# Optimization experiments

Hardware: AMD Instinct MI355X
Metric: run time of the kernel (lower is better)

Reference implementation:

```python
import jax, jax.numpy as jnp
import numpy as np

B, S, D = 2, 2048, 1024
H, DK = 16, 64  # num_heads, key_dim (value_dim defaults to key_dim)


def setup_inputs() -> dict:
    key = jax.random.key(0)
    ks = jax.random.split(key, 11)
    init = lambda k, shape, fan_in: jax.random.uniform(
        k, shape, jnp.float32, -1.0, 1.0) * (1.0 / np.sqrt(fan_in))
    return {
        "query": jax.random.normal(ks[0], (B, S, D), jnp.float32),
        "key": jax.random.normal(ks[1], (B, S, D), jnp.float32),
        "value": jax.random.normal(ks[2], (B, S, D), jnp.float32),
        "Wq": init(ks[3], (D, H, DK), D),
        "bq": jnp.zeros((H, DK), jnp.float32),
        "Wk": init(ks[4], (D, H, DK), D),
        "bk": jnp.zeros((H, DK), jnp.float32),
        "Wv": init(ks[5], (D, H, DK), D),
        "bv": jnp.zeros((H, DK), jnp.float32),
        "Wo": init(ks[6], (H, DK, D), H * DK),
        "bo": jnp.zeros((D,), jnp.float32),
    }


def reference(query, key, value, Wq, bq, Wk, bk, Wv, bv, Wo, bo):
    # QKV projections: abc,cde->abde (EinsumDense with bias on (H, DK))
    q = jnp.einsum("bsd,dhk->bshk", query, Wq) + bq  # [B,S,H,DK]
    k = jnp.einsum("bsd,dhk->bshk", key, Wk) + bk
    v = jnp.einsum("bsd,dhk->bshk", value, Wv) + bv
    # Keras scales the query before the dot product
    q = q * (1.0 / jnp.sqrt(jnp.asarray(DK, q.dtype)))
    # aecd,abcd->acbe : [B,H,Sq,Sk]
    scores = jnp.einsum("bqhk,bshk->bhqs", q, k)
    probs = jax.nn.softmax(scores, axis=-1)
    # acbe,aecd->abcd : [B,Sq,H,DK]
    attn = jnp.einsum("bhqs,bshk->bqhk", probs, v)
    # output projection: abcd,cde->abe
    out = jnp.einsum("bqhk,hkd->bqd", attn, Wo) + bo  # [B,S,D]
    return out
```

## Files before the change

### kernel.cpp

```cpp
#include <hip/hip_runtime.h>
#include <hip/hip_bf16.h>
#include <stdint.h>
#include <stddef.h>


typedef __bf16 bf16;
typedef __attribute__((ext_vector_type(4))) bf16 bf16x4;
typedef __attribute__((ext_vector_type(8))) bf16 bf16x8;
typedef __attribute__((ext_vector_type(4))) float f32x4;
typedef __attribute__((ext_vector_type(16))) float f32x16;
typedef __attribute__((ext_vector_type(2))) unsigned int uint2v;

#define DEVINL static __device__ __forceinline__

DEVINL void gload_lds16(const void* g, void* l) {
  __builtin_amdgcn_global_load_lds(
      (const __attribute__((address_space(1))) void*)g,
      (__attribute__((address_space(3))) void*)l, 16, 0, 0);
}

DEVINL f32x4 mfma16(bf16x8 a, bf16x8 b, f32x4 c) {
  return __builtin_amdgcn_mfma_f32_16x16x32_bf16(a, b, c, 0, 0, 0);
}
DEVINL f32x16 mfma32(bf16x8 a, bf16x8 b, f32x16 c) {
  return __builtin_amdgcn_mfma_f32_32x32x16_bf16(a, b, c, 0, 0, 0);
}
DEVINL float fexp2(float x) {
  float r;
  asm("v_exp_f32 %0, %1" : "=v"(r) : "v"(x));
  return r;
}
DEVINL unsigned pack2(float lo, float hi) {
  union { bf16 h[2]; unsigned u; } t;
  t.h[0] = (bf16)lo; t.h[1] = (bf16)hi;
  return t.u;
}
DEVINL bf16x8 mk8(unsigned a, unsigned b, unsigned c, unsigned d) {
  union { unsigned u[4]; bf16x8 v; } t;
  t.u[0] = a; t.u[1] = b; t.u[2] = c; t.u[3] = d;
  return t.v;
}

__global__ __launch_bounds__(256) void wt_kernel(
    const float* __restrict__ w0, const float* __restrict__ w1,
    const float* __restrict__ w2, const float* __restrict__ w3,
    bf16* __restrict__ out) {
  __shared__ float tile[64 * 65];
  int t = blockIdx.y;
  const float* w = (t == 0) ? w0 : (t == 1) ? w1 : (t == 2) ? w2 : w3;
  bf16* o = out + (size_t)t * 1024 * 1024;
  int tb = blockIdx.x;
  int k0 = (tb >> 4) * 64, n0 = (tb & 15) * 64;
  int c = threadIdx.x & 63, r0 = threadIdx.x >> 6;
  for (int r = r0; r < 64; r += 4)
    tile[r * 65 + c] = w[(size_t)(k0 + r) * 1024 + n0 + c];
  __syncthreads();
  for (int r = r0; r < 64; r += 4)
    o[(size_t)(n0 + r) * 1024 + k0 + c] = (bf16)tile[c * 65 + r];
}

__global__ __launch_bounds__(256) void cvt_kernel(
    const float* __restrict__ q, const float* __restrict__ k,
    const float* __restrict__ v, bf16* __restrict__ out) {
  int z = blockIdx.y;
  const float* src = (z == 0) ? q : (z == 1) ? k : v;
  size_t off = ((size_t)blockIdx.x * 256 + threadIdx.x) * 8;
  f32x4 a = *(const f32x4*)(src + off);
  f32x4 b = *(const f32x4*)(src + off + 4);
  bf16x8 h;
#pragma unroll
  for (int j = 0; j < 4; ++j) { h[j] = (bf16)a[j]; h[4 + j] = (bf16)b[j]; }
  *(bf16x8*)(out + (size_t)z * 4194304 + off) = h;
}

__global__ __launch_bounds__(256) void gemm_qkv(
    const bf16* __restrict__ Abf, const bf16* __restrict__ Wt,
    const float* __restrict__ bq, const float* __restrict__ bk,
    const float* __restrict__ bv,
    bf16* __restrict__ outQ, bf16* __restrict__ outK, bf16* __restrict__ Vt) {
  int z = blockIdx.z;
  const bf16* A    = Abf + (size_t)z * 4194304;
  const bf16* Wz   = Wt + (size_t)z * 1024 * 1024;
  const float* bia = (z == 0) ? bq : (z == 1) ? bk : bv;
  float scale      = (z == 0) ? 0.18033688011112042f : 1.0f;

  __shared__ bf16 As[2][128 * 32];
  __shared__ bf16 Bs[2][128 * 32];

  int m0 = blockIdx.x * 128, n0 = blockIdx.y * 128;
  int tid = threadIdx.x, w = tid >> 6, l = tid & 63;
  int wm = (w >> 1) * 64, wn = (w & 1) * 64;
  int c16 = l & 15, g = l >> 4;
  int rsw = (c16 >> 1) & 3;

  int brow0 = (w * 2 + 0) * 16 + (l >> 2);
  int brow1 = (w * 2 + 1) * 16 + (l >> 2);
  int bk0 = ((l & 3) ^ ((brow0 >> 1) & 3)) * 8;
  int bk1 = ((l & 3) ^ ((brow1 >> 1) & 3)) * 8;

  f32x4 acc[4][4] = {};

#define STAGE_QKV(buf, kt)                                                   \
  do {                                                                       \
    gload_lds16(A + (size_t)(m0 + brow0) * 1024 + (kt) + bk0,                \
                (char*)As[buf] + (w * 2 + 0) * 1024 + l * 16);               \
    gload_lds16(A + (size_t)(m0 + brow1) * 1024 + (kt) + bk1,                \
                (char*)As[buf] + (w * 2 + 1) * 1024 + l * 16);               \
    gload_lds16(Wz + (size_t)(n0 + brow0) * 1024 + (kt) + bk0,               \
                (char*)Bs[buf] + (w * 2 + 0) * 1024 + l * 16);               \
    gload_lds16(Wz + (size_t)(n0 + brow1) * 1024 + (kt) + bk1,               \
                (char*)Bs[buf] + (w * 2 + 1) * 1024 + l * 16);               \
  } while (0)

  STAGE_QKV(0, 0);
  __syncthreads();

  int cur = 0;
  for (int kt = 0; kt < 1024; kt += 32) {
    if (kt < 992) STAGE_QKV(cur ^ 1, kt + 32);
    bf16x8 af[4], bfr[4];
#pragma unroll
    for (int mt = 0; mt < 4; ++mt)
      af[mt] = *(const bf16x8*)&As[cur][(wm + mt * 16 + c16) * 32 + ((g ^ rsw) * 8)];
#pragma unroll
    for (int nt = 0; nt < 4; ++nt)
      bfr[nt] = *(const bf16x8*)&Bs[cur][(wn + nt * 16 + c16) * 32 + ((g ^ rsw) * 8)];
#pragma unroll
    for (int mt = 0; mt < 4; ++mt)
#pragma unroll
      for (int nt = 0; nt < 4; ++nt)
        acc[mt][nt] = mfma16(af[mt], bfr[nt], acc[mt][nt]);
    __syncthreads();
    cur ^= 1;
  }
#undef STAGE_QKV

  if (z < 2) {
    bf16* Cout = (z == 0) ? outQ : outK;
#pragma unroll
    for (int mt = 0; mt < 4; ++mt)
#pragma unroll
      for (int nt = 0; nt < 4; ++nt) {
        int n = n0 + wn + nt * 16 + c16;
        float bb = bia[n];
#pragma unroll
        for (int r = 0; r < 4; ++r) {
          int m = m0 + wm + mt * 16 + g * 4 + r;
          Cout[(size_t)m * 1024 + n] = (bf16)((acc[mt][nt][r] + bb) * scale);
        }
      }
  } else {
#pragma unroll
    for (int mt = 0; mt < 4; ++mt)
#pragma unroll
      for (int nt = 0; nt < 4; ++nt) {
        int n = n0 + wn + nt * 16 + c16;
        float bb = bia[n];
        int m = m0 + wm + mt * 16 + g * 4;
        int b = m >> 11, s = m & 2047;
        bf16x4 v;
#pragma unroll
        for (int r = 0; r < 4; ++r) v[r] = (bf16)(acc[mt][nt][r] + bb);
        *(bf16x4*)&Vt[((size_t)(b * 16 + (n >> 6)) * 64 + (n & 63)) * 2048 + s] = v;
      }
  }
}

__global__ __launch_bounds__(256) void flash_kernel(
    const bf16* __restrict__ Qp, const bf16* __restrict__ Kp,
    const bf16* __restrict__ Vt, bf16* __restrict__ AO) {
  __shared__ __align__(16) bf16 Ks[2][64 * 64];
  __shared__ __align__(16) bf16 Vs[2][64 * 64];

  int orig = blockIdx.x;
  int wg = (orig & 7) * 64 + (orig >> 3);
  int bh = wg >> 4, qb = wg & 15;
  int b = bh >> 4, h = bh & 15;
  int tid = threadIdx.x, w = tid >> 6, l = tid & 63;
  int lo5 = l & 31, g = l >> 5;
  int q0 = qb * 128 + w * 32;

  const bf16* qptr = Qp + (size_t)(b * 2048 + q0 + lo5) * 1024 + h * 64 + g * 8;
  bf16x8 qf0 = *(const bf16x8*)(qptr + 0);
  bf16x8 qf1 = *(const bf16x8*)(qptr + 16);
  bf16x8 qf2 = *(const bf16x8*)(qptr + 32);
  bf16x8 qf3 = *(const bf16x8*)(qptr + 48);

  const bf16* kbase = Kp + (size_t)(b * 2048) * 1024 + h * 64;
  const bf16* vbase = Vt + (size_t)bh * 64 * 2048;

  int u0 = w * 64 + l;
  int u1 = (4 + w) * 64 + l;
  int r0s = u0 >> 3, c0s = (u0 & 7) ^ (r0s & 7);
  int r1s = u1 >> 3, c1s = (u1 & 7) ^ (r1s & 7);

#define STAGE(buf, s0)                                                          \
  do {                                                                          \
    gload_lds16(kbase + (size_t)((s0) + r0s) * 1024 + c0s * 8,                  \
                (bf16*)Ks[buf] + u0 * 8);                                       \
    gload_lds16(kbase + (size_t)((s0) + r1s) * 1024 + c1s * 8,                  \
                (bf16*)Ks[buf] + u1 * 8);                                       \
    gload_lds16(vbase + (size_t)r0s * 2048 + (s0) + c0s * 8,                    \
                (bf16*)Vs[buf] + u0 * 8);                                       \
    gload_lds16(vbase + (size_t)r1s * 2048 + (s0) + c1s * 8,                    \
                (bf16*)Vs[buf] + u1 * 8);                                       \
  } while (0)

#define LDSK(cp, nt, kt) \
  (*(const bf16x8*)&cp[(((nt)*32 + lo5) << 6) + (((((kt)*2 + g)) ^ (lo5 & 7)) << 3)])
#define LDSV(cp, dt, st) \
  (*(const bf16x8*)&cp[(((dt)*32 + lo5) << 6) + (((((st)*2 + g)) ^ (lo5 & 7)) << 3)])

  f32x16 o0 = {}, o1 = {};
  float ps0 = 0.f, ps1 = 0.f, ps2 = 0.f, ps3 = 0.f;

  STAGE(0, 0);
  int cur = 0;
  for (int t = 0; t < 32; ++t) {
    if (t < 31) {
      STAGE(cur ^ 1, (t + 1) * 64);
      asm volatile("s_waitcnt vmcnt(4)" ::: "memory");
    } else {
      asm volatile("s_waitcnt vmcnt(0)" ::: "memory");
    }
    __builtin_amdgcn_s_barrier();
    __builtin_amdgcn_sched_barrier(0);
    const bf16* kc = Ks[cur];
    const bf16* vc = Vs[cur];

    f32x16 sv = {};
    __builtin_amdgcn_s_setprio(1);
    sv = mfma32(LDSK(kc, 0, 0), qf0, sv);
    sv = mfma32(LDSK(kc, 0, 1), qf1, sv);
    sv = mfma32(LDSK(kc, 0, 2), qf2, sv);
    sv = mfma32(LDSK(kc, 0, 3), qf3, sv);
    __builtin_amdgcn_s_setprio(0);
    float p[16];
#pragma unroll
    for (int r = 0; r < 16; ++r) p[r] = fexp2(sv[r]);
    ps0 += p[0] + p[4] + p[8] + p[12];
    ps1 += p[1] + p[5] + p[9] + p[13];
    ps2 += p[2] + p[6] + p[10] + p[14];
    ps3 += p[3] + p[7] + p[11] + p[15];
    unsigned pw0 = pack2(p[0], p[1]), pw1 = pack2(p[2], p[3]);
    unsigned pw2 = pack2(p[4], p[5]), pw3 = pack2(p[6], p[7]);
    unsigned pw4 = pack2(p[8], p[9]), pw5 = pack2(p[10], p[11]);
    unsigned pw6 = pack2(p[12], p[13]), pw7 = pack2(p[14], p[15]);
    uint2v a02 = __builtin_amdgcn_permlane32_swap(pw0, pw2, false, false);
    uint2v a13 = __builtin_amdgcn_permlane32_swap(pw1, pw3, false, false);
    uint2v a46 = __builtin_amdgcn_permlane32_swap(pw4, pw6, false, false);
    uint2v a57 = __builtin_amdgcn_permlane32_swap(pw5, pw7, false, false);
    bf16x8 pa0 = mk8(a02.x, a13.x, a02.y, a13.y);
    bf16x8 pa1 = mk8(a46.x, a57.x, a46.y, a57.y);

    f32x16 sw = {};
    __builtin_amdgcn_s_setprio(1);
    sw = mfma32(LDSK(kc, 1, 0), qf0, sw);
    sw = mfma32(LDSK(kc, 1, 1), qf1, sw);
    sw = mfma32(LDSK(kc, 1, 2), qf2, sw);
    sw = mfma32(LDSK(kc, 1, 3), qf3, sw);
    __builtin_amdgcn_s_setprio(0);
#pragma unroll
    for (int r = 0; r < 16; ++r) p[r] = fexp2(sw[r]);
    ps0 += p[0] + p[4] + p[8] + p[12];
    ps1 += p[1] + p[5] + p[9] + p[13];
    ps2 += p[2] + p[6] + p[10] + p[14];
    ps3 += p[3] + p[7] + p[11] + p[15];
    pw0 = pack2(p[0], p[1]); pw1 = pack2(p[2], p[3]);
    pw2 = pack2(p[4], p[5]); pw3 = pack2(p[6], p[7]);
    pw4 = pack2(p[8], p[9]); pw5 = pack2(p[10], p[11]);
    pw6 = pack2(p[12], p[13]); pw7 = pack2(p[14], p[15]);
    a02 = __builtin_amdgcn_permlane32_swap(pw0, pw2, false, false);
    a13 = __builtin_amdgcn_permlane32_swap(pw1, pw3, false, false);
    a46 = __builtin_amdgcn_permlane32_swap(pw4, pw6, false, false);
    a57 = __builtin_amdgcn_permlane32_swap(pw5, pw7, false, false);
    bf16x8 pb0 = mk8(a02.x, a13.x, a02.y, a13.y);
    bf16x8 pb1 = mk8(a46.x, a57.x, a46.y, a57.y);

    __builtin_amdgcn_s_setprio(1);
    o0 = mfma32(pa0, LDSV(vc, 0, 0), o0);
    o1 = mfma32(pa0, LDSV(vc, 1, 0), o1);
    o0 = mfma32(pa1, LDSV(vc, 0, 1), o0);
    o1 = mfma32(pa1, LDSV(vc, 1, 1), o1);
    o0 = mfma32(pb0, LDSV(vc, 0, 2), o0);
    o1 = mfma32(pb0, LDSV(vc, 1, 2), o1);
    o0 = mfma32(pb1, LDSV(vc, 0, 3), o0);
    o1 = mfma32(pb1, LDSV(vc, 1, 3), o1);
    __builtin_amdgcn_s_setprio(0);

    __builtin_amdgcn_sched_barrier(0);
    __builtin_amdgcn_s_barrier();
    cur ^= 1;
  }
#undef STAGE
#undef LDSK
#undef LDSV

  float plsum = (ps0 + ps1) + (ps2 + ps3);
  float tot = plsum + __shfl_xor(plsum, 32);

#pragma unroll
  for (int r = 0; r < 16; ++r) {
    int qr = (r & 3) + 8 * (r >> 2) + 4 * g;
    float inv = 1.0f / __shfl(tot, qr);
    bf16* op = AO + (size_t)(b * 2048 + q0 + qr) * 1024 + h * 64 + lo5;
    op[0]  = (bf16)(o0[r] * inv);
    op[32] = (bf16)(o1[r] * inv);
  }
}

__global__ __launch_bounds__(256) void gemm_o(
    const bf16* __restrict__ A, const bf16* __restrict__ Wt3,
    const float* __restrict__ bo, float* __restrict__ C) {
  __shared__ bf16 As[2][128 * 32];
  __shared__ bf16 Bs[2][128 * 32];
  int m0 = blockIdx.x * 128, n0 = blockIdx.y * 128;
  int tid = threadIdx.x, w = tid >> 6, l = tid & 63;
  int wm = (w >> 1) * 64, wn = (w & 1) * 64;
  int c16 = l & 15, g = l >> 4;
  int rsw = (c16 >> 1) & 3;

  int brow0 = (w * 2 + 0) * 16 + (l >> 2);
  int brow1 = (w * 2 + 1) * 16 + (l >> 2);
  int bk0 = ((l & 3) ^ ((brow0 >> 1) & 3)) * 8;
  int bk1 = ((l & 3) ^ ((brow1 >> 1) & 3)) * 8;

  f32x4 acc[4][4] = {};

#define STAGE_O(buf, kt)                                                     \
  do {                                                                       \
    gload_lds16(A + (size_t)(m0 + brow0) * 1024 + (kt) + bk0,                \
                (char*)As[buf] + (w * 2 + 0) * 1024 + l * 16);               \
    gload_lds16(A + (size_t)(m0 + brow1) * 1024 + (kt) + bk1,                \
                (char*)As[buf] + (w * 2 + 1) * 1024 + l * 16);               \
    gload_lds16(Wt3 + (size_t)(n0 + brow0) * 1024 + (kt) + bk0,              \
                (char*)Bs[buf] + (w * 2 + 0) * 1024 + l * 16);               \
    gload_lds16(Wt3 + (size_t)(n0 + brow1) * 1024 + (kt) + bk1,              \
                (char*)Bs[buf] + (w * 2 + 1) * 1024 + l * 16);               \
  } while (0)

  STAGE_O(0, 0);
  __syncthreads();

  int cur = 0;
  for (int kt = 0; kt < 1024; kt += 32) {
    if (kt < 992) STAGE_O(cur ^ 1, kt + 32);
    bf16x8 af[4], bfr[4];
#pragma unroll
    for (int mt = 0; mt < 4; ++mt)
      af[mt] = *(const bf16x8*)&As[cur][(wm + mt * 16 + c16) * 32 + ((g ^ rsw) * 8)];
#pragma unroll
    for (int nt = 0; nt < 4; ++nt)
      bfr[nt] = *(const bf16x8*)&Bs[cur][(wn + nt * 16 + c16) * 32 + ((g ^ rsw) * 8)];
#pragma unroll
    for (int mt = 0; mt < 4; ++mt)
#pragma unroll
      for (int nt = 0; nt < 4; ++nt)
        acc[mt][nt] = mfma16(af[mt], bfr[nt], acc[mt][nt]);
    __syncthreads();
    cur ^= 1;
  }
#undef STAGE_O

#pragma unroll
  for (int mt = 0; mt < 4; ++mt)
#pragma unroll
    for (int nt = 0; nt < 4; ++nt) {
      int n = n0 + wn + nt * 16 + c16;
      float bb = bo[n];
#pragma unroll
      for (int r = 0; r < 4; ++r) {
        int m = m0 + wm + mt * 16 + g * 4 + r;
        C[(size_t)m * 1024 + n] = acc[mt][nt][r] + bb;
      }
    }
}

extern "C" void kernel_launch(void* const* d_in, const int* in_sizes, int n_in,
                              void* d_out, int out_size, void* d_ws, size_t ws_size,
                              hipStream_t stream) {
  const float* query = (const float*)d_in[0];
  const float* key_  = (const float*)d_in[1];
  const float* value = (const float*)d_in[2];
  const float* Wq = (const float*)d_in[3];
  const float* bq = (const float*)d_in[4];
  const float* Wk = (const float*)d_in[5];
  const float* bk = (const float*)d_in[6];
  const float* Wv = (const float*)d_in[7];
  const float* bv = (const float*)d_in[8];
  const float* Wo = (const float*)d_in[9];
  const float* bo = (const float*)d_in[10];
  float* out = (float*)d_out;

  char* ws = (char*)d_ws;
  const size_t MB = 1024 * 1024;
  bf16* Wt  = (bf16*)(ws);
  bf16* Abf = (bf16*)(ws + 8 * MB);
  bf16* Qp  = (bf16*)(ws + 32 * MB);
  bf16* Kp  = (bf16*)(ws + 40 * MB);
  bf16* Vt  = (bf16*)(ws + 48 * MB);
  bf16* AO  = (bf16*)(ws + 8 * MB);

  dim3 blk(256);
  wt_kernel<<<dim3(256, 4), blk, 0, stream>>>(Wq, Wk, Wv, Wo, Wt);
  cvt_kernel<<<dim3(2048, 3), blk, 0, stream>>>(query, key_, value, Abf);
  gemm_qkv<<<dim3(32, 8, 3), blk, 0, stream>>>(Abf, Wt, bq, bk, bv, Qp, Kp, Vt);
  flash_kernel<<<dim3(512), blk, 0, stream>>>(Qp, Kp, Vt, AO);
  gemm_o<<<dim3(32, 8), blk, 0, stream>>>(AO, Wt + (size_t)3 * 1024 * 1024, bo, out);
}
```

Baseline: 132.1 us.

## Split KV range across wave pairs in flash kernel and halve gemm_o M tile

The flash kernel now assigns 64 queries per block instead of 128, and each pair of waves splits every 64-key tile into two 32-key halves. The partial outputs and row sums are combined through LDS at the end, and the grid doubles to 1024 blocks. The output-projection GEMM tile shrinks from 128 to 64 rows, also doubling its block count. Both changes aim to fill more CUs on the 256-CU part, at the cost of an extra LDS reduction and more redundant K/V and weight loads per query.

```diff
diff --git a/kernel.cpp b/kernel.cpp
--- a/kernel.cpp
+++ b/kernel.cpp
@@ -173,12 +173,13 @@
   __shared__ __align__(16) bf16 Vs[2][64 * 64];
 
   int orig = blockIdx.x;
-  int wg = (orig & 7) * 64 + (orig >> 3);
-  int bh = wg >> 4, qb = wg & 15;
+  int wg = (orig & 7) * 128 + (orig >> 3);
+  int bh = wg >> 5, qb = wg & 31;
   int b = bh >> 4, h = bh & 15;
   int tid = threadIdx.x, w = tid >> 6, l = tid & 63;
   int lo5 = l & 31, g = l >> 5;
-  int q0 = qb * 128 + w * 32;
+  int qhalf = w >> 1, kvhalf = w & 1;
+  int q0 = qb * 64 + qhalf * 32;
 
   const bf16* qptr = Qp + (size_t)(b * 2048 + q0 + lo5) * 1024 + h * 64 + g * 8;
   bf16x8 qf0 = *(const bf16x8*)(qptr + 0);
@@ -230,10 +231,10 @@
 
     f32x16 sv = {};
     __builtin_amdgcn_s_setprio(1);
-    sv = mfma32(LDSK(kc, 0, 0), qf0, sv);
-    sv = mfma32(LDSK(kc, 0, 1), qf1, sv);
-    sv = mfma32(LDSK(kc, 0, 2), qf2, sv);
-    sv = mfma32(LDSK(kc, 0, 3), qf3, sv);
+    sv = mfma32(LDSK(kc, kvhalf, 0), qf0, sv);
+    sv = mfma32(LDSK(kc, kvhalf, 1), qf1, sv);
+    sv = mfma32(LDSK(kc, kvhalf, 2), qf2, sv);
+    sv = mfma32(LDSK(kc, kvhalf, 3), qf3, sv);
     __builtin_amdgcn_s_setprio(0);
     float p[16];
 #pragma unroll
@@ -253,39 +254,11 @@
     bf16x8 pa0 = mk8(a02.x, a13.x, a02.y, a13.y);
     bf16x8 pa1 = mk8(a46.x, a57.x, a46.y, a57.y);
 
-    f32x16 sw = {};
     __builtin_amdgcn_s_setprio(1);
-    sw = mfma32(LDSK(kc, 1, 0), qf0, sw);
-    sw = mfma32(LDSK(kc, 1, 1), qf1, sw);
-    sw = mfma32(LDSK(kc, 1, 2), qf2, sw);
-    sw = mfma32(LDSK(kc, 1, 3), qf3, sw);
-    __builtin_amdgcn_s_setprio(0);
-#pragma unroll
-    for (int r = 0; r < 16; ++r) p[r] = fexp2(sw[r]);
-    ps0 += p[0] + p[4] + p[8] + p[12];
-    ps1 += p[1] + p[5] + p[9] + p[13];
-    ps2 += p[2] + p[6] + p[10] + p[14];
-    ps3 += p[3] + p[7] + p[11] + p[15];
-    pw0 = pack2(p[0], p[1]); pw1 = pack2(p[2], p[3]);
-    pw2 = pack2(p[4], p[5]); pw3 = pack2(p[6], p[7]);
-    pw4 = pack2(p[8], p[9]); pw5 = pack2(p[10], p[11]);
-    pw6 = pack2(p[12], p[13]); pw7 = pack2(p[14], p[15]);
-    a02 = __builtin_amdgcn_permlane32_swap(pw0, pw2, false, false);
-    a13 = __builtin_amdgcn_permlane32_swap(pw1, pw3, false, false);
-    a46 = __builtin_amdgcn_permlane32_swap(pw4, pw6, false, false);
-    a57 = __builtin_amdgcn_permlane32_swap(pw5, pw7, false, false);
-    bf16x8 pb0 = mk8(a02.x, a13.x, a02.y, a13.y);
-    bf16x8 pb1 = mk8(a46.x, a57.x, a46.y, a57.y);
-
-    __builtin_amdgcn_s_setprio(1);
-    o0 = mfma32(pa0, LDSV(vc, 0, 0), o0);
-    o1 = mfma32(pa0, LDSV(vc, 1, 0), o1);
-    o0 = mfma32(pa1, LDSV(vc, 0, 1), o0);
-    o1 = mfma32(pa1, LDSV(vc, 1, 1), o1);
-    o0 = mfma32(pb0, LDSV(vc, 0, 2), o0);
-    o1 = mfma32(pb0, LDSV(vc, 1, 2), o1);
-    o0 = mfma32(pb1, LDSV(vc, 0, 3), o0);
-    o1 = mfma32(pb1, LDSV(vc, 1, 3), o1);
+    o0 = mfma32(pa0, LDSV(vc, 0, kvhalf * 2 + 0), o0);
+    o1 = mfma32(pa0, LDSV(vc, 1, kvhalf * 2 + 0), o1);
+    o0 = mfma32(pa1, LDSV(vc, 0, kvhalf * 2 + 1), o0);
+    o1 = mfma32(pa1, LDSV(vc, 1, kvhalf * 2 + 1), o1);
     __builtin_amdgcn_s_setprio(0);
 
     __builtin_amdgcn_sched_barrier(0);
@@ -299,40 +272,67 @@
   float plsum = (ps0 + ps1) + (ps2 + ps3);
   float tot = plsum + __shfl_xor(plsum, 32);
 
-#pragma unroll
-  for (int r = 0; r < 16; ++r) {
-    int qr = (r & 3) + 8 * (r >> 2) + 4 * g;
-    float inv = 1.0f / __shfl(tot, qr);
-    bf16* op = AO + (size_t)(b * 2048 + q0 + qr) * 1024 + h * 64 + lo5;
-    op[0]  = (bf16)(o0[r] * inv);
-    op[32] = (bf16)(o1[r] * inv);
+  float* ored = (float*)Ks;
+  float* dred = (float*)Vs;
+  if (kvhalf) {
+    float* dst = ored + (qhalf * 64 + l) * 32;
+#pragma unroll
+    for (int c = 0; c < 8; ++c) {
+      int base = ((c + l) & 7) * 4;
+#pragma unroll
+      for (int j = 0; j < 4; ++j)
+        dst[base + j] = (c < 4) ? o0[c * 4 + j] : o1[(c - 4) * 4 + j];
+    }
+    dred[qhalf * 64 + l] = tot;
+  }
+  __syncthreads();
+  if (!kvhalf) {
+    const float* src = ored + (qhalf * 64 + l) * 32;
+#pragma unroll
+    for (int c = 0; c < 8; ++c) {
+      int base = ((c + l) & 7) * 4;
+#pragma unroll
+      for (int j = 0; j < 4; ++j) {
+        float v = src[base + j];
+        if (c < 4) o0[c * 4 + j] += v; else o1[(c - 4) * 4 + j] += v;
+      }
+    }
+    float tot2 = tot + dred[qhalf * 64 + l];
+#pragma unroll
+    for (int r = 0; r < 16; ++r) {
+      int qr = (r & 3) + 8 * (r >> 2) + 4 * g;
+      float inv = 1.0f / __shfl(tot2, qr);
+      bf16* op = AO + (size_t)(b * 2048 + q0 + qr) * 1024 + h * 64 + lo5;
+      op[0]  = (bf16)(o0[r] * inv);
+      op[32] = (bf16)(o1[r] * inv);
+    }
   }
 }
 
 __global__ __launch_bounds__(256) void gemm_o(
     const bf16* __restrict__ A, const bf16* __restrict__ Wt3,
     const float* __restrict__ bo, float* __restrict__ C) {
-  __shared__ bf16 As[2][128 * 32];
+  __shared__ bf16 As[2][64 * 32];
   __shared__ bf16 Bs[2][128 * 32];
-  int m0 = blockIdx.x * 128, n0 = blockIdx.y * 128;
+  int m0 = blockIdx.x * 64, n0 = blockIdx.y * 128;
   int tid = threadIdx.x, w = tid >> 6, l = tid & 63;
-  int wm = (w >> 1) * 64, wn = (w & 1) * 64;
+  int wm = (w >> 1) * 32, wn = (w & 1) * 64;
   int c16 = l & 15, g = l >> 4;
   int rsw = (c16 >> 1) & 3;
 
+  int arow = tid >> 2, akc = tid & 3;
+  int asrc = (akc ^ ((arow >> 1) & 3)) * 8;
   int brow0 = (w * 2 + 0) * 16 + (l >> 2);
   int brow1 = (w * 2 + 1) * 16 + (l >> 2);
   int bk0 = ((l & 3) ^ ((brow0 >> 1) & 3)) * 8;
   int bk1 = ((l & 3) ^ ((brow1 >> 1) & 3)) * 8;
 
-  f32x4 acc[4][4] = {};
+  f32x4 acc[2][4] = {};
 
 #define STAGE_O(buf, kt)                                                     \
   do {                                                                       \
-    gload_lds16(A + (size_t)(m0 + brow0) * 1024 + (kt) + bk0,                \
-                (char*)As[buf] + (w * 2 + 0) * 1024 + l * 16);               \
-    gload_lds16(A + (size_t)(m0 + brow1) * 1024 + (kt) + bk1,                \
-                (char*)As[buf] + (w * 2 + 1) * 1024 + l * 16);               \
+    gload_lds16(A + (size_t)(m0 + arow) * 1024 + (kt) + asrc,                \
+                (char*)As[buf] + tid * 16);                                  \
     gload_lds16(Wt3 + (size_t)(n0 + brow0) * 1024 + (kt) + bk0,              \
                 (char*)Bs[buf] + (w * 2 + 0) * 1024 + l * 16);               \
     gload_lds16(Wt3 + (size_t)(n0 + brow1) * 1024 + (kt) + bk1,              \
@@ -345,15 +345,15 @@
   int cur = 0;
   for (int kt = 0; kt < 1024; kt += 32) {
     if (kt < 992) STAGE_O(cur ^ 1, kt + 32);
-    bf16x8 af[4], bfr[4];
-#pragma unroll
-    for (int mt = 0; mt < 4; ++mt)
+    bf16x8 af[2], bfr[4];
+#pragma unroll
+    for (int mt = 0; mt < 2; ++mt)
       af[mt] = *(const bf16x8*)&As[cur][(wm + mt * 16 + c16) * 32 + ((g ^ rsw) * 8)];
 #pragma unroll
     for (int nt = 0; nt < 4; ++nt)
       bfr[nt] = *(const bf16x8*)&Bs[cur][(wn + nt * 16 + c16) * 32 + ((g ^ rsw) * 8)];
 #pragma unroll
-    for (int mt = 0; mt < 4; ++mt)
+    for (int mt = 0; mt < 2; ++mt)
 #pragma unroll
       for (int nt = 0; nt < 4; ++nt)
         acc[mt][nt] = mfma16(af[mt], bfr[nt], acc[mt][nt]);
@@ -363,7 +363,7 @@
 #undef STAGE_O
 
 #pragma unroll
-  for (int mt = 0; mt < 4; ++mt)
+  for (int mt = 0; mt < 2; ++mt)
 #pragma unroll
     for (int nt = 0; nt < 4; ++nt) {
       int n = n0 + wn + nt * 16 + c16;
@@ -405,6 +405,6 @@
   wt_kernel<<<dim3(256, 4), blk, 0, stream>>>(Wq, Wk, Wv, Wo, Wt);
   cvt_kernel<<<dim3(2048, 3), blk, 0, stream>>>(query, key_, value, Abf);
   gemm_qkv<<<dim3(32, 8, 3), blk, 0, stream>>>(Abf, Wt, bq, bk, bv, Qp, Kp, Vt);
-  flash_kernel<<<dim3(512), blk, 0, stream>>>(Qp, Kp, Vt, AO);
-  gemm_o<<<dim3(32, 8), blk, 0, stream>>>(AO, Wt + (size_t)3 * 1024 * 1024, bo, out);
-}
+  flash_kernel<<<dim3(1024), blk, 0, stream>>>(Qp, Kp, Vt, AO);
+  gemm_o<<<dim3(64, 8), blk, 0, stream>>>(AO, Wt + (size_t)3 * 1024 * 1024, bo, out);
+}
```

After: 149.3 us. 13.0% more time.

## Deepen flash K/V ring to 4 buffers, fuse prep kernels, shrink gemm_o tile

Applied to the files above, without the earlier changes.

The flash kernel now uses a 4-deep K/V LDS ring that prefetches two tiles ahead, replacing the double buffer. This drops the trailing barrier so there is one barrier per iteration, aiming to hide global load latency. The weight-transpose and input-conversion kernels are merged into one launch to cut launch overhead. gemm_o uses 64-row M tiles, doubling its grid for better CU occupancy. In exchange, flash uses twice as much LDS, and gemm_o reuses each B tile less.

```diff
diff --git a/kernel.cpp b/kernel.cpp
--- a/kernel.cpp
+++ b/kernel.cpp
@@ -41,36 +41,38 @@
   return t.v;
 }
 
-__global__ __launch_bounds__(256) void wt_kernel(
+__global__ __launch_bounds__(256) void prep_kernel(
+    const float* __restrict__ q, const float* __restrict__ k,
+    const float* __restrict__ v,
     const float* __restrict__ w0, const float* __restrict__ w1,
     const float* __restrict__ w2, const float* __restrict__ w3,
-    bf16* __restrict__ out) {
+    bf16* __restrict__ Abf, bf16* __restrict__ Wt) {
   __shared__ float tile[64 * 65];
-  int t = blockIdx.y;
-  const float* w = (t == 0) ? w0 : (t == 1) ? w1 : (t == 2) ? w2 : w3;
-  bf16* o = out + (size_t)t * 1024 * 1024;
-  int tb = blockIdx.x;
-  int k0 = (tb >> 4) * 64, n0 = (tb & 15) * 64;
-  int c = threadIdx.x & 63, r0 = threadIdx.x >> 6;
-  for (int r = r0; r < 64; r += 4)
-    tile[r * 65 + c] = w[(size_t)(k0 + r) * 1024 + n0 + c];
-  __syncthreads();
-  for (int r = r0; r < 64; r += 4)
-    o[(size_t)(n0 + r) * 1024 + k0 + c] = (bf16)tile[c * 65 + r];
-}
-
-__global__ __launch_bounds__(256) void cvt_kernel(
-    const float* __restrict__ q, const float* __restrict__ k,
-    const float* __restrict__ v, bf16* __restrict__ out) {
-  int z = blockIdx.y;
-  const float* src = (z == 0) ? q : (z == 1) ? k : v;
-  size_t off = ((size_t)blockIdx.x * 256 + threadIdx.x) * 8;
-  f32x4 a = *(const f32x4*)(src + off);
-  f32x4 b = *(const f32x4*)(src + off + 4);
-  bf16x8 h;
-#pragma unroll
-  for (int j = 0; j < 4; ++j) { h[j] = (bf16)a[j]; h[4 + j] = (bf16)b[j]; }
-  *(bf16x8*)(out + (size_t)z * 4194304 + off) = h;
+  int bx = blockIdx.x;
+  if (bx < 6144) {
+    int z = bx >> 11, blk = bx & 2047;
+    const float* src = (z == 0) ? q : (z == 1) ? k : v;
+    size_t off = ((size_t)blk * 256 + threadIdx.x) * 8;
+    f32x4 a = *(const f32x4*)(src + off);
+    f32x4 b = *(const f32x4*)(src + off + 4);
+    bf16x8 h;
+#pragma unroll
+    for (int j = 0; j < 4; ++j) { h[j] = (bf16)a[j]; h[4 + j] = (bf16)b[j]; }
+    *(bf16x8*)(Abf + (size_t)z * 4194304 + off) = h;
+  } else {
+    int tb = bx - 6144;
+    int t = tb >> 8;
+    tb &= 255;
+    const float* w = (t == 0) ? w0 : (t == 1) ? w1 : (t == 2) ? w2 : w3;
+    bf16* o = Wt + (size_t)t * 1024 * 1024;
+    int k0 = (tb >> 4) * 64, n0 = (tb & 15) * 64;
+    int c = threadIdx.x & 63, r0 = threadIdx.x >> 6;
+    for (int r = r0; r < 64; r += 4)
+      tile[r * 65 + c] = w[(size_t)(k0 + r) * 1024 + n0 + c];
+    __syncthreads();
+    for (int r = r0; r < 64; r += 4)
+      o[(size_t)(n0 + r) * 1024 + k0 + c] = (bf16)tile[c * 65 + r];
+  }
 }
 
 __global__ __launch_bounds__(256) void gemm_qkv(
@@ -169,8 +171,8 @@
 __global__ __launch_bounds__(256) void flash_kernel(
     const bf16* __restrict__ Qp, const bf16* __restrict__ Kp,
     const bf16* __restrict__ Vt, bf16* __restrict__ AO) {
-  __shared__ __align__(16) bf16 Ks[2][64 * 64];
-  __shared__ __align__(16) bf16 Vs[2][64 * 64];
+  __shared__ __align__(16) bf16 Ks[4][64 * 64];
+  __shared__ __align__(16) bf16 Vs[4][64 * 64];
 
   int orig = blockIdx.x;
   int wg = (orig & 7) * 64 + (orig >> 3);
@@ -215,18 +217,20 @@
   float ps0 = 0.f, ps1 = 0.f, ps2 = 0.f, ps3 = 0.f;
 
   STAGE(0, 0);
-  int cur = 0;
+  STAGE(1, 64);
   for (int t = 0; t < 32; ++t) {
-    if (t < 31) {
-      STAGE(cur ^ 1, (t + 1) * 64);
+    if (t < 30) {
+      STAGE((t + 2) & 3, (t + 2) * 64);
+      asm volatile("s_waitcnt vmcnt(8)" ::: "memory");
+    } else if (t == 30) {
       asm volatile("s_waitcnt vmcnt(4)" ::: "memory");
     } else {
       asm volatile("s_waitcnt vmcnt(0)" ::: "memory");
     }
     __builtin_amdgcn_s_barrier();
     __builtin_amdgcn_sched_barrier(0);
-    const bf16* kc = Ks[cur];
-    const bf16* vc = Vs[cur];
+    const bf16* kc = Ks[t & 3];
+    const bf16* vc = Vs[t & 3];
 
     f32x16 sv = {};
     __builtin_amdgcn_s_setprio(1);
@@ -287,10 +291,6 @@
     o0 = mfma32(pb1, LDSV(vc, 0, 3), o0);
     o1 = mfma32(pb1, LDSV(vc, 1, 3), o1);
     __builtin_amdgcn_s_setprio(0);
-
-    __builtin_amdgcn_sched_barrier(0);
-    __builtin_amdgcn_s_barrier();
-    cur ^= 1;
   }
 #undef STAGE
 #undef LDSK
@@ -312,27 +312,27 @@
 __global__ __launch_bounds__(256) void gemm_o(
     const bf16* __restrict__ A, const bf16* __restrict__ Wt3,
     const float* __restrict__ bo, float* __restrict__ C) {
-  __shared__ bf16 As[2][128 * 32];
+  __shared__ bf16 As[2][64 * 32];
   __shared__ bf16 Bs[2][128 * 32];
-  int m0 = blockIdx.x * 128, n0 = blockIdx.y * 128;
+  int m0 = blockIdx.x * 64, n0 = blockIdx.y * 128;
   int tid = threadIdx.x, w = tid >> 6, l = tid & 63;
-  int wm = (w >> 1) * 64, wn = (w & 1) * 64;
+  int wm = (w >> 1) * 32, wn = (w & 1) * 64;
   int c16 = l & 15, g = l >> 4;
   int rsw = (c16 >> 1) & 3;
 
+  int arow = tid >> 2, akc = tid & 3;
+  int asrc = (akc ^ ((arow >> 1) & 3)) * 8;
   int brow0 = (w * 2 + 0) * 16 + (l >> 2);
   int brow1 = (w * 2 + 1) * 16 + (l >> 2);
   int bk0 = ((l & 3) ^ ((brow0 >> 1) & 3)) * 8;
   int bk1 = ((l & 3) ^ ((brow1 >> 1) & 3)) * 8;
 
-  f32x4 acc[4][4] = {};
+  f32x4 acc[2][4] = {};
 
 #define STAGE_O(buf, kt)                                                     \
   do {                                                                       \
-    gload_lds16(A + (size_t)(m0 + brow0) * 1024 + (kt) + bk0,                \
-                (char*)As[buf] + (w * 2 + 0) * 1024 + l * 16);               \
-    gload_lds16(A + (size_t)(m0 + brow1) * 1024 + (kt) + bk1,                \
-                (char*)As[buf] + (w * 2 + 1) * 1024 + l * 16);               \
+    gload_lds16(A + (size_t)(m0 + arow) * 1024 + (kt) + asrc,                \
+                (char*)As[buf] + tid * 16);                                  \
     gload_lds16(Wt3 + (size_t)(n0 + brow0) * 1024 + (kt) + bk0,              \
                 (char*)Bs[buf] + (w * 2 + 0) * 1024 + l * 16);               \
     gload_lds16(Wt3 + (size_t)(n0 + brow1) * 1024 + (kt) + bk1,              \
@@ -345,15 +345,15 @@
   int cur = 0;
   for (int kt = 0; kt < 1024; kt += 32) {
     if (kt < 992) STAGE_O(cur ^ 1, kt + 32);
-    bf16x8 af[4], bfr[4];
-#pragma unroll
-    for (int mt = 0; mt < 4; ++mt)
+    bf16x8 af[2], bfr[4];
+#pragma unroll
+    for (int mt = 0; mt < 2; ++mt)
       af[mt] = *(const bf16x8*)&As[cur][(wm + mt * 16 + c16) * 32 + ((g ^ rsw) * 8)];
 #pragma unroll
     for (int nt = 0; nt < 4; ++nt)
       bfr[nt] = *(const bf16x8*)&Bs[cur][(wn + nt * 16 + c16) * 32 + ((g ^ rsw) * 8)];
 #pragma unroll
-    for (int mt = 0; mt < 4; ++mt)
+    for (int mt = 0; mt < 2; ++mt)
 #pragma unroll
       for (int nt = 0; nt < 4; ++nt)
         acc[mt][nt] = mfma16(af[mt], bfr[nt], acc[mt][nt]);
@@ -363,7 +363,7 @@
 #undef STAGE_O
 
 #pragma unroll
-  for (int mt = 0; mt < 4; ++mt)
+  for (int mt = 0; mt < 2; ++mt)
 #pragma unroll
     for (int nt = 0; nt < 4; ++nt) {
       int n = n0 + wn + nt * 16 + c16;
@@ -402,9 +402,9 @@
   bf16* AO  = (bf16*)(ws + 8 * MB);
 
   dim3 blk(256);
-  wt_kernel<<<dim3(256, 4), blk, 0, stream>>>(Wq, Wk, Wv, Wo, Wt);
-  cvt_kernel<<<dim3(2048, 3), blk, 0, stream>>>(query, key_, value, Abf);
+  prep_kernel<<<dim3(7168), blk, 0, stream>>>(query, key_, value,
+                                              Wq, Wk, Wv, Wo, Abf, Wt);
   gemm_qkv<<<dim3(32, 8, 3), blk, 0, stream>>>(Abf, Wt, bq, bk, bv, Qp, Kp, Vt);
   flash_kernel<<<dim3(512), blk, 0, stream>>>(Qp, Kp, Vt, AO);
-  gemm_o<<<dim3(32, 8), blk, 0, stream>>>(AO, Wt + (size_t)3 * 1024 * 1024, bo, out);
-}
+  gemm_o<<<dim3(64, 8), blk, 0, stream>>>(AO, Wt + (size_t)3 * 1024 * 1024, bo, out);
+}
```

Result: no change. 132.8 us (+0.5%).
